# Optimization experiments

Hardware: AMD Instinct MI355X
Metric: run time of the kernel (lower is better)

## Reference

```python
import jax, jax.numpy as jnp
import numpy as np
from jax import lax

EPS = 1e-5
K, S = 7, 4  # patch size / stride, hard-coded in the torch module


def _bn(x, g, b):
    # inference BN with running_mean=0, running_var=1
    return x * (g / np.sqrt(1.0 + EPS)).reshape(1, -1, 1, 1) + b.reshape(1, -1, 1, 1)


def _conv2d(x, w, groups=1, pad=0):
    return lax.conv_general_dilated(
        x, w, (1, 1), [(pad, pad), (pad, pad)],
        dimension_numbers=("NCHW", "OIHW", "NCHW"), feature_group_count=groups)


def _dsconv(x, dw_w, g1, b1, pw_w, g2, b2):
    c_in = x.shape[1]
    y = jax.nn.relu(_bn(_conv2d(x, dw_w, groups=c_in, pad=1), g1, b1))
    y = jax.nn.relu(_bn(_conv2d(y, pw_w, groups=1, pad=0), g2, b2))
    return y


def _unfold(x, nph, npw):
    # torch .unfold(2,K,S).unfold(3,K,S) -> [N,C,nph,npw,K,K]
    idx_h = jnp.arange(nph)[:, None] * S + jnp.arange(K)[None, :]  # [nph,K]
    idx_w = jnp.arange(npw)[:, None] * S + jnp.arange(K)[None, :]  # [npw,K]
    p = x[:, :, idx_h, :]            # [N,C,nph,K,W]
    p = p[:, :, :, :, idx_w]         # [N,C,nph,K,npw,K]
    return p.transpose(0, 1, 2, 4, 3, 5)  # [N,C,nph,npw,K,K]


def setup_inputs() -> dict:
    key = jax.random.key(0)
    ks = jax.random.split(key, 16)
    N, C, H, W = 8, 128, 128, 128
    sc = lambda *s: 1.0 / np.sqrt(np.prod(s[1:])) if len(s) > 1 else 0.02
    d = {
        "exemplar": jax.random.normal(ks[0], (N, C, H, W), jnp.float32),
        "query": jax.random.normal(ks[1], (N, C, H, W), jnp.float32),
        "w_conv_e": jax.random.normal(ks[2], (C, C), jnp.float32) * (1.0 / np.sqrt(C)),
        "w_gate1": jax.random.normal(ks[3], (1, C), jnp.float32) * (1.0 / np.sqrt(C)),
        "w_gate2": jax.random.normal(ks[4], (1, C), jnp.float32) * (1.0 / np.sqrt(C)),
        "dw1_w": jax.random.normal(ks[5], (C, 1, 3, 3), jnp.float32) * (1.0 / 3.0),
        "bn1a_g": jnp.ones((C,), jnp.float32), "bn1a_b": jnp.zeros((C,), jnp.float32),
        "pw1_w": jax.random.normal(ks[6], (C, C, 1, 1), jnp.float32) * (1.0 / np.sqrt(C)),
        "bn1b_g": jnp.ones((C,), jnp.float32), "bn1b_b": jnp.zeros((C,), jnp.float32),
        "dwf_w": jax.random.normal(ks[7], (2 * C, 1, 3, 3), jnp.float32) * (1.0 / 3.0),
        "bnfa_g": jnp.ones((2 * C,), jnp.float32), "bnfa_b": jnp.zeros((2 * C,), jnp.float32),
        "pwf_w": jax.random.normal(ks[8], (C, 2 * C, 1, 1), jnp.float32) * (1.0 / np.sqrt(2 * C)),
        "bnfb_g": jnp.ones((C,), jnp.float32), "bnfb_b": jnp.zeros((C,), jnp.float32),
    }
    return d


def reference(exemplar, query, w_conv_e, w_gate1, w_gate2,
              dw1_w, bn1a_g, bn1a_b, pw1_w, bn1b_g, bn1b_b,
              dwf_w, bnfa_g, bnfa_b, pwf_w, bnfb_g, bnfb_b):
    N, C, H, W = query.shape
    nph = (H - K) // S + 1
    npw = (W - K) // S + 1
    npatch = nph * npw
    D = K * K  # 49

    ex_p = _unfold(exemplar, nph, npw)  # [N,C,nph,npw,K,K]
    q_p = _unfold(query, nph, npw)
    # faithful to torch: raw row-major reinterpretation [N,C,nph,npw,K,K] -> [N*npatch, C, D]
    ex_flat = ex_p.reshape(N * npatch, C, D)
    q_flat = q_p.reshape(N * npatch, C, D)

    ex_corr = jnp.einsum("oc,bcd->bod", w_conv_e, ex_flat)       # conv1d k=1
    A = jnp.einsum("bcd,bce->bde", ex_corr, q_flat)              # [B,D,D]
    A1 = jax.nn.softmax(A, axis=1)
    B2 = jax.nn.softmax(A, axis=2)                               # = softmax(A^T, dim=1) transposed back
    query_att = jnp.einsum("bcd,bde->bce", ex_flat, A1)          # [B,C,D]
    exemplar_att = jnp.einsum("bce,bde->bcd", q_flat, B2)        # [B,C,D]

    def recon(att):
        a = att.reshape(N, nph, npw, C, K, K)
        a = a.transpose(0, 3, 1, 4, 2, 5).reshape(N, C, nph * K, npw * K)
        return a[:, :, :H, :W]

    query_att = recon(query_att)
    exemplar_att = recon(exemplar_att)

    ex_mask = jax.nn.sigmoid(jnp.einsum("oc,nchw->nohw", w_gate1, exemplar_att))
    exemplar_att = exemplar_att * ex_mask
    exemplar_out = _dsconv(exemplar_att + exemplar, dw1_w, bn1a_g, bn1a_b, pw1_w, bn1b_g, bn1b_b)

    q_mask = jax.nn.sigmoid(jnp.einsum("oc,nchw->nohw", w_gate2, query_att))
    query_att = query_att * q_mask
    query_out = _dsconv(query_att + query, dw1_w, bn1a_g, bn1a_b, pw1_w, bn1b_g, bn1b_b)

    pred = _dsconv(jnp.concatenate([exemplar_out, query_out], axis=1),
                   dwf_w, bnfa_g, bnfa_b, pwf_w, bnfb_g, bnfb_b)
    return pred
```

## Files before the change

kernel.cpp:

```cpp
#include <hip/hip_runtime.h>
#include <hip/hip_bf16.h>

#define NN 8
#define CC 128
#define HH 128
#define WW 128
#define HWP (HH*WW)
#define KK 7
#define DD 49
#define NPH 31
#define NPATCH 961
#define PHN 19
#define PAD 52
#define PP2 (PAD*PAD)

typedef __attribute__((ext_vector_type(8))) short bf16x8;
typedef __attribute__((ext_vector_type(4))) float f32x4;
typedef __attribute__((ext_vector_type(4))) unsigned short us4;

__device__ __forceinline__ unsigned short f2bf(float f) {
    unsigned u = __builtin_bit_cast(unsigned, f);
    return (unsigned short)((u + 0x7FFFu + ((u >> 16) & 1u)) >> 16);
}

__global__ __launch_bounds__(512, 4) void attn_kernel(
    const float* __restrict__ ex_g, const float* __restrict__ q_g,
    const float* __restrict__ Wce, const float* __restrict__ wg1,
    const float* __restrict__ wg2,
    float* __restrict__ xe, float* __restrict__ xq)
{
    __shared__ float s_ex[CC*PAD];
    __shared__ float s_q [CC*PAD];
    __shared__ float s_scr[CC*PAD];
    __shared__ float s_m1[PAD], s_l1[PAD], s_m2[PAD], s_l2[PAD];
    __shared__ float s_g1[PAD], s_g2[PAD], s_me[PAD], s_mq[PAD];

    const int t  = threadIdx.x;
    const int n  = blockIdx.y;
    const int ph = blockIdx.x / PHN;
    const int pw = blockIdx.x % PHN;
    const int pp = (ph * NPH + pw) * CC;

    const float* exn = ex_g + (size_t)n * CC * HWP;
    const float* qn  = q_g  + (size_t)n * CC * HWP;

    #pragma unroll
    for (int ii = 0; ii < 2; ++ii) {
        const int i  = t + ii*512;
        const int c2 = i >> 3, kh = i & 7;
        const int rem  = pp + c2;
        const int c_u  = rem / NPATCH;
        const int p_u  = rem - c_u * NPATCH;
        const int ph_u = p_u / NPH;
        const int pw_u = p_u - ph_u * NPH;
        float* de = &s_ex[c2*PAD + kh*KK];
        if (kh < KK) {
            const float* se = exn + ((c_u*HH + ph_u*4 + kh)*WW + pw_u*4);
            const float4 e4 = *(const float4*)se;
            const float2 e2 = *(const float2*)(se + 4);
            const float  e1 = se[6];
            de[0]=e4.x; de[1]=e4.y; de[2]=e4.z; de[3]=e4.w;
            de[4]=e2.x; de[5]=e2.y; de[6]=e1;
        } else {
            de[0]=0.f; de[1]=0.f; de[2]=0.f;
        }
    }
    __syncthreads();

    if (t >= 64 && t < 480) {
        const int t2 = t - 64;
        const int eg_o = t2 / 13, eg_d = t2 - (t2/13)*13;
        const int o0 = eg_o*4, d0 = eg_d*4;
        float ac[4][4];
        #pragma unroll
        for (int i = 0; i < 4; ++i)
            #pragma unroll
            for (int j = 0; j < 4; ++j) ac[i][j] = 0.f;
        for (int k = 0; k < CC; k += 4) {
            float xm[4][4];
            #pragma unroll
            for (int kk = 0; kk < 4; ++kk) {
                float4 xv = *(const float4*)&s_ex[(k+kk)*PAD + d0];
                xm[kk][0]=xv.x; xm[kk][1]=xv.y; xm[kk][2]=xv.z; xm[kk][3]=xv.w;
            }
            #pragma unroll
            for (int i = 0; i < 4; ++i) {
                float4 wv = *(const float4*)&Wce[(o0+i)*CC + k];
                float wr[4] = {wv.x, wv.y, wv.z, wv.w};
                #pragma unroll
                for (int kk = 0; kk < 4; ++kk)
                    #pragma unroll
                    for (int j = 0; j < 4; ++j)
                        ac[i][j] = fmaf(wr[kk], xm[kk][j], ac[i][j]);
            }
        }
        #pragma unroll
        for (int i = 0; i < 4; ++i)
            *(float4*)&s_scr[(o0+i)*PAD + d0] =
                make_float4(ac[i][0], ac[i][1], ac[i][2], ac[i][3]);
    } else if (t < 64) {
        #pragma unroll 4
        for (int jj = 0; jj < 16; ++jj) {
            const int i  = t + jj*64;
            const int c2 = i >> 3, kh = i & 7;
            const int rem  = pp + c2;
            const int c_u  = rem / NPATCH;
            const int p_u  = rem - c_u * NPATCH;
            const int ph_u = p_u / NPH;
            const int pw_u = p_u - ph_u * NPH;
            float* dq = &s_q[c2*PAD + kh*KK];
            if (kh < KK) {
                const float* sq = qn + ((c_u*HH + ph_u*4 + kh)*WW + pw_u*4);
                const float4 q4 = *(const float4*)sq;
                const float2 q2 = *(const float2*)(sq + 4);
                const float  q1 = sq[6];
                dq[0]=q4.x; dq[1]=q4.y; dq[2]=q4.z; dq[3]=q4.w;
                dq[4]=q2.x; dq[5]=q2.y; dq[6]=q1;
            } else {
                dq[0]=0.f; dq[1]=0.f; dq[2]=0.f;
            }
        }
    }
    __syncthreads();

    float aa[4][2];
    int ad0 = 0, ae0 = 0;
    if (t < 338) {
        int dg = t % 13, eg = t / 13;
        ad0 = dg*4; ae0 = eg*2;
        #pragma unroll
        for (int i = 0; i < 4; ++i) { aa[i][0] = 0.f; aa[i][1] = 0.f; }
        #pragma unroll 4
        for (int k = 0; k < CC; ++k) {
            float4 ev = *(const float4*)&s_scr[k*PAD + ad0];
            float2 qv = *(const float2*)&s_q [k*PAD + ae0];
            #pragma unroll
            for (int i = 0; i < 4; ++i) {
                float e = (i==0)?ev.x:(i==1)?ev.y:(i==2)?ev.z:ev.w;
                aa[i][0] = fmaf(e, qv.x, aa[i][0]);
                aa[i][1] = fmaf(e, qv.y, aa[i][1]);
            }
        }
    } else if (t >= 352 && t < 352 + DD) {
        int e = t - 352;
        float acc = 0.f;
        for (int c = 0; c < CC; ++c) acc = fmaf(wg1[c], s_q[c*PAD + e], acc);
        s_g1[e] = acc;
    } else if (t >= 416 && t < 416 + DD) {
        int d = t - 416;
        float acc = 0.f;
        for (int c = 0; c < CC; ++c) acc = fmaf(wg2[c], s_ex[c*PAD + d], acc);
        s_g2[d] = acc;
    }
    __syncthreads();
    if (t < 338) {
        #pragma unroll
        for (int i = 0; i < 4; ++i)
            *(float2*)&s_scr[(ad0+i)*PAD + ae0] = make_float2(aa[i][0], aa[i][1]);
    }
    __syncthreads();

    {
        const int sub  = t & 3;
        const int line = (t >> 2) & 63;
        const int lo   = sub * 13;
        float v[13];
        if (t < 256) {
            if (line < DD) {
                #pragma unroll
                for (int j = 0; j < 13; ++j) {
                    int d = lo + j;
                    v[j] = (d < DD) ? s_scr[d*PAD + line] : -1e30f;
                }
                float m = v[0];
                #pragma unroll
                for (int j = 1; j < 13; ++j) m = fmaxf(m, v[j]);
                m = fmaxf(m, __shfl_xor(m, 1));
                m = fmaxf(m, __shfl_xor(m, 2));
                float l = 0.f;
                #pragma unroll
                for (int j = 0; j < 13; ++j) l += __expf(v[j] - m);
                l += __shfl_xor(l, 1);
                l += __shfl_xor(l, 2);
                if (sub == 0) { s_m1[line] = m; s_l1[line] = 1.f / l; }
            } else if (line < PAD && sub == 0) { s_m1[line] = 0.f; s_l1[line] = 0.f; }
        } else {
            if (line < DD) {
                #pragma unroll
                for (int j = 0; j < 13; ++j) {
                    int e = lo + j;
                    v[j] = (e < DD) ? s_scr[line*PAD + e] : -1e30f;
                }
                float m = v[0];
                #pragma unroll
                for (int j = 1; j < 13; ++j) m = fmaxf(m, v[j]);
                m = fmaxf(m, __shfl_xor(m, 1));
                m = fmaxf(m, __shfl_xor(m, 2));
                float l = 0.f;
                #pragma unroll
                for (int j = 0; j < 13; ++j) l += __expf(v[j] - m);
                l += __shfl_xor(l, 1);
                l += __shfl_xor(l, 2);
                if (sub == 0) { s_m2[line] = m; s_l2[line] = 1.f / l; }
            } else if (line < PAD && sub == 0) { s_m2[line] = 0.f; s_l2[line] = 0.f; }
        }
    }
    __syncthreads();

    float* P1  = s_scr + PP2;
    float* P2T = s_scr;
    {
        float p2buf[6]; int nv = 0;
        for (int i = t; i < PP2; i += 512) {
            int d = i / PAD, e = i - d*PAD;
            float a = s_scr[i];
            P1[i] = __expf(a - s_m1[e]) * s_l1[e];
            p2buf[nv++] = __expf(a - s_m2[d]) * s_l2[d];
        }
        __syncthreads();
        nv = 0;
        for (int i = t; i < PP2; i += 512) {
            int d = i / PAD, e = i - d*PAD;
            P2T[e*PAD + d] = p2buf[nv++];
        }
    }
    __syncthreads();

    float ae_[4][4], aq_[4][4];
    int c0 = 0, x0 = 0;
    if (t < 416) {
        int cg = t / 13, xg = t - (t/13)*13;
        c0 = cg*4; x0 = xg*4;
        #pragma unroll
        for (int i = 0; i < 4; ++i)
            #pragma unroll
            for (int j = 0; j < 4; ++j) { ae_[i][j] = 0.f; aq_[i][j] = 0.f; }
        for (int k = 0; k < 48; k += 4) {
            float qm[4][4], xm[4][4], p1m[4][4], p2m[4][4];
            #pragma unroll
            for (int i = 0; i < 4; ++i) {
                float4 qv = *(const float4*)&s_q [(c0+i)*PAD + k];
                float4 xv = *(const float4*)&s_ex[(c0+i)*PAD + k];
                qm[i][0]=qv.x; qm[i][1]=qv.y; qm[i][2]=qv.z; qm[i][3]=qv.w;
                xm[i][0]=xv.x; xm[i][1]=xv.y; xm[i][2]=xv.z; xm[i][3]=xv.w;
            }
            #pragma unroll
            for (int kk = 0; kk < 4; ++kk) {
                float4 p1 = *(const float4*)&P1 [(k+kk)*PAD + x0];
                float4 p2 = *(const float4*)&P2T[(k+kk)*PAD + x0];
                p1m[kk][0]=p1.x; p1m[kk][1]=p1.y; p1m[kk][2]=p1.z; p1m[kk][3]=p1.w;
                p2m[kk][0]=p2.x; p2m[kk][1]=p2.y; p2m[kk][2]=p2.z; p2m[kk][3]=p2.w;
            }
            #pragma unroll
            for (int kk = 0; kk < 4; ++kk)
                #pragma unroll
                for (int i = 0; i < 4; ++i)
                    #pragma unroll
                    for (int j = 0; j < 4; ++j) {
                        ae_[i][j] = fmaf(qm[i][kk], p2m[kk][j], ae_[i][j]);
                        aq_[i][j] = fmaf(xm[i][kk], p1m[kk][j], aq_[i][j]);
                    }
        }
        {
            const int k = 48;
            float p1r[4], p2r[4];
            #pragma unroll
            for (int j = 0; j < 4; ++j) { p1r[j] = P1 [k*PAD + x0 + j];
                                          p2r[j] = P2T[k*PAD + x0 + j]; }
            #pragma unroll
            for (int i = 0; i < 4; ++i) {
                float qv = s_q [(c0+i)*PAD + k];
                float xv = s_ex[(c0+i)*PAD + k];
                #pragma unroll
                for (int j = 0; j < 4; ++j) {
                    ae_[i][j] = fmaf(qv, p2r[j], ae_[i][j]);
                    aq_[i][j] = fmaf(xv, p1r[j], aq_[i][j]);
                }
            }
        }
    } else {
        const int u = t - 416;
        if (u < DD) {
            float a1 = 0.f;
            for (int e = 0; e < DD; ++e) a1 = fmaf(s_g1[e], P2T[e*PAD + u], a1);
            s_me[u] = 1.f / (1.f + __expf(-a1));
            if (u < 2) {
                const int e2 = DD - 2 + u;
                float a2 = 0.f;
                for (int d = 0; d < DD; ++d) a2 = fmaf(s_g2[d], P1[d*PAD + e2], a2);
                s_mq[e2] = 1.f / (1.f + __expf(-a2));
            }
        } else {
            const int e2 = u - DD;
            float a2 = 0.f;
            for (int d = 0; d < DD; ++d) a2 = fmaf(s_g2[d], P1[d*PAD + e2], a2);
            s_mq[e2] = 1.f / (1.f + __expf(-a2));
        }
    }
    __syncthreads();
    if (t < 416) {
        #pragma unroll
        for (int i = 0; i < 4; ++i) {
            *(float4*)&s_ex[(c0+i)*PAD + x0] =
                make_float4(ae_[i][0], ae_[i][1], ae_[i][2], ae_[i][3]);
            *(float4*)&s_q [(c0+i)*PAD + x0] =
                make_float4(aq_[i][0], aq_[i][1], aq_[i][2], aq_[i][3]);
        }
    }
    __syncthreads();

    {
        const size_t nbase = (size_t)n * CC * HWP;
        const int hb = ph*KK, wb = pw*KK;
        const int wlim = (WW - wb) < KK ? (WW - wb) : KK;
        #pragma unroll
        for (int ii = 0; ii < 2; ++ii) {
            const int i  = t + ii*512;
            const int c  = i >> 3, kh = i & 7;
            const int h  = hb + kh;
            if (kh < KK && h < HH) {
                const int li = (c*HH + h)*WW + wb;
                const float* sxe = &s_ex[c*PAD + kh*KK];
                const float* sxq = &s_q [c*PAD + kh*KK];
                if (wlim == KK) {
                    #pragma unroll
                    for (int kw = 0; kw < KK; ++kw) {
                        const int d = kh*KK + kw;
                        xe[nbase + li + kw] = sxe[kw]*s_me[d] + exn[li + kw];
                        xq[nbase + li + kw] = sxq[kw]*s_mq[d] + qn [li + kw];
                    }
                } else {
                    for (int kw = 0; kw < wlim; ++kw) {
                        const int d = kh*KK + kw;
                        xe[nbase + li + kw] = sxe[kw]*s_me[d] + exn[li + kw];
                        xq[nbase + li + kw] = sxq[kw]*s_mq[d] + qn [li + kw];
                    }
                }
            }
        }
    }
}

__global__ __launch_bounds__(256) void dw2_kernel(
    const float* __restrict__ xA, unsigned short* __restrict__ yA,
    const float* __restrict__ xB, unsigned short* __restrict__ yB,
    const float* __restrict__ wdw, const float* __restrict__ g,
    const float* __restrict__ b, int CoutTot, int coffA, int coffB)
{
    int bid = blockIdx.x;
    int sel = bid >> 12;
    int idx = (bid & 4095) * 256 + threadIdx.x;
    const float* x = sel ? xB : xA;
    unsigned short* y = sel ? yB : yA;
    int coff          = sel ? coffB : coffA;

    int w4 = (idx & 31) * 4;
    int h4 = ((idx >> 5) & 31) * 4;
    int nc = idx >> 10;
    int c  = nc & 127;
    int n  = nc >> 7;

    const float* wp = wdw + (coff + c) * 9;
    float wr[9];
    #pragma unroll
    for (int i = 0; i < 9; ++i) wr[i] = wp[i];

    const float* base = x + (size_t)nc * HWP;
    float acc[4][4];
    #pragma unroll
    for (int i = 0; i < 4; ++i)
        #pragma unroll
        for (int j = 0; j < 4; ++j) acc[i][j] = 0.f;

    #pragma unroll
    for (int r = 0; r < 6; ++r) {
        int hh = h4 - 1 + r;
        if (hh >= 0 && hh < HH) {
            const float* row = base + hh * WW + w4;
            float4 v = *(const float4*)row;
            float e[6];
            e[0] = (w4 > 0)   ? row[-1] : 0.f;
            e[1] = v.x; e[2] = v.y; e[3] = v.z; e[4] = v.w;
            e[5] = (w4 < 124) ? row[4]  : 0.f;
            int ilo = r - 2 > 0 ? r - 2 : 0;
            int ihi = r < 3 ? r : 3;
            for (int i = ilo; i <= ihi; ++i) {
                int j = r - i;
                float wa = wr[j*3], wb = wr[j*3+1], wc = wr[j*3+2];
                acc[i][0] += wa*e[0] + wb*e[1] + wc*e[2];
                acc[i][1] += wa*e[1] + wb*e[2] + wc*e[3];
                acc[i][2] += wa*e[2] + wb*e[3] + wc*e[4];
                acc[i][3] += wa*e[3] + wb*e[4] + wc*e[5];
            }
        }
    }
    const float rs = 0.99999500003749968f;
    float sc = g[coff + c] * rs, bi = b[coff + c];
    unsigned short* outp = y + (((size_t)n * CoutTot + coff + c) * HH + h4) * WW + w4;
    #pragma unroll
    for (int i = 0; i < 4; ++i) {
        us4 o;
        o[0] = f2bf(fmaxf(acc[i][0] * sc + bi, 0.f));
        o[1] = f2bf(fmaxf(acc[i][1] * sc + bi, 0.f));
        o[2] = f2bf(fmaxf(acc[i][2] * sc + bi, 0.f));
        o[3] = f2bf(fmaxf(acc[i][3] * sc + bi, 0.f));
        *(us4*)(outp + i * WW) = o;
    }
}

#define ZSTR 56

__global__ __launch_bounds__(256, 2) void pw_mfma_kernel(
    const unsigned short* __restrict__ zA, float* __restrict__ outA,
    const unsigned short* __restrict__ zB, float* __restrict__ outB,
    const float* __restrict__ Wp, const float* __restrict__ g,
    const float* __restrict__ b, int Cin)
{
    __shared__ unsigned short s_w[128*ZSTR];
    __shared__ unsigned short s_z[128*ZSTR];

    const int t  = threadIdx.x;
    const int n  = blockIdx.y;
    const int p0 = blockIdx.x * 128;
    const unsigned short* z = blockIdx.z ? zB : zA;
    float* out              = blockIdx.z ? outB : outA;

    const int wave = t >> 6, lane = t & 63;
    const int wo  = (wave & 1) * 64;
    const int wp_ = (wave >> 1) * 64;
    const int lm  = lane & 15, lq = lane >> 4;

    f32x4 acc[4][4];
    #pragma unroll
    for (int i = 0; i < 4; ++i)
        #pragma unroll
        for (int j = 0; j < 4; ++j)
            #pragma unroll
            for (int r = 0; r < 4; ++r) acc[i][j][r] = 0.f;

    const unsigned short* zn = z + (size_t)n * Cin * HWP;

    for (int kb = 0; kb < Cin; kb += 32) {
        {
            int o = t >> 1, cb = (t & 1) * 16;
            const float* wrow = Wp + o * Cin + kb + cb;
            unsigned short* dst = s_w + o * ZSTR + cb;
            #pragma unroll
            for (int i = 0; i < 16; i += 4) {
                float4 v = *(const float4*)(wrow + i);
                dst[i+0] = f2bf(v.x); dst[i+1] = f2bf(v.y);
                dst[i+2] = f2bf(v.z); dst[i+3] = f2bf(v.w);
            }
        }
        {
            int cc = t & 31, pxg = (t >> 5) * 16;
            const unsigned short* src = zn + (size_t)(kb + cc) * HWP + p0 + pxg;
            uint4 a = *(const uint4*)src;
            uint4 b2 = *(const uint4*)(src + 8);
            unsigned v[8] = {a.x, a.y, a.z, a.w, b2.x, b2.y, b2.z, b2.w};
            #pragma unroll
            for (int i = 0; i < 8; ++i) {
                s_z[(pxg + 2*i    ) * ZSTR + cc] = (unsigned short)(v[i] & 0xffffu);
                s_z[(pxg + 2*i + 1) * ZSTR + cc] = (unsigned short)(v[i] >> 16);
            }
        }
        __syncthreads();

        bf16x8 af[4], bfv[4];
        #pragma unroll
        for (int i = 0; i < 4; ++i)
            af[i] = *(const bf16x8*)&s_w[(wo + i*16 + lm) * ZSTR + lq*8];
        #pragma unroll
        for (int j = 0; j < 4; ++j)
            bfv[j] = *(const bf16x8*)&s_z[(wp_ + j*16 + lm) * ZSTR + lq*8];
        #pragma unroll
        for (int i = 0; i < 4; ++i)
            #pragma unroll
            for (int j = 0; j < 4; ++j)
                acc[i][j] = __builtin_amdgcn_mfma_f32_16x16x32_bf16(
                    af[i], bfv[j], acc[i][j], 0, 0, 0);
        __syncthreads();
    }

    const float rs = 0.99999500003749968f;
    float* on = out + (size_t)n * 128 * HWP;
    #pragma unroll
    for (int i = 0; i < 4; ++i) {
        #pragma unroll
        for (int r = 0; r < 4; ++r) {
            int o = wo + i*16 + lq*4 + r;
            float sc = g[o] * rs, bi = b[o];
            #pragma unroll
            for (int j = 0; j < 4; ++j) {
                int px = wp_ + j*16 + lm;
                on[(size_t)o * HWP + p0 + px] =
                    fmaxf(acc[i][j][r] * sc + bi, 0.f);
            }
        }
    }
}

extern "C" void kernel_launch(void* const* d_in, const int* in_sizes, int n_in,
                              void* d_out, int out_size, void* d_ws, size_t ws_size,
                              hipStream_t stream) {
    const float* exemplar = (const float*)d_in[0];
    const float* query    = (const float*)d_in[1];
    const float* w_conv_e = (const float*)d_in[2];
    const float* w_gate1  = (const float*)d_in[3];
    const float* w_gate2  = (const float*)d_in[4];
    const float* dw1_w    = (const float*)d_in[5];
    const float* bn1a_g   = (const float*)d_in[6];
    const float* bn1a_b   = (const float*)d_in[7];
    const float* pw1_w    = (const float*)d_in[8];
    const float* bn1b_g   = (const float*)d_in[9];
    const float* bn1b_b   = (const float*)d_in[10];
    const float* dwf_w    = (const float*)d_in[11];
    const float* bnfa_g   = (const float*)d_in[12];
    const float* bnfa_b   = (const float*)d_in[13];
    const float* pwf_w    = (const float*)d_in[14];
    const float* bnfb_g   = (const float*)d_in[15];
    const float* bnfb_b   = (const float*)d_in[16];

    float* out = (float*)d_out;
    float* ws  = (float*)d_ws;
    const size_t SZ = (size_t)NN * CC * HWP;
    float* bufA = ws;
    float* bufB = ws + SZ;
    unsigned short* zE  = (unsigned short*)(ws + 2*SZ);
    unsigned short* zQ  = zE + SZ;
    unsigned short* T16 = (unsigned short*)(ws + 3*SZ);

    attn_kernel<<<dim3(PHN * PHN, NN), 512, 0, stream>>>(
        exemplar, query, w_conv_e, w_gate1, w_gate2, bufA, bufB);

    dw2_kernel<<<8192, 256, 0, stream>>>(bufA, zE, bufB, zQ,
                                         dw1_w, bn1a_g, bn1a_b, 128, 0, 0);

    pw_mfma_kernel<<<dim3(128, NN, 2), 256, 0, stream>>>(
        zE, bufA, zQ, bufB, pw1_w, bn1b_g, bn1b_b, 128);

    dw2_kernel<<<8192, 256, 0, stream>>>(bufA, T16, bufB, T16,
                                         dwf_w, bnfa_g, bnfa_b, 256, 0, 128);

    pw_mfma_kernel<<<dim3(128, NN, 1), 256, 0, stream>>>(
        T16, out, (const unsigned short*)nullptr, (float*)nullptr,
        pwf_w, bnfb_g, bnfb_b, 256);
}
```

Baseline: 669.3 us.

## Compute patch attention products with bf16 MFMA and fold gate masks into stores

Replaces the scalar fp32 4x4 register-tiled products of the exemplar/query patches with the softmax matrices in the attention kernel with bf16 16x16x32 MFMA instructions. The operands are converted to bf16 in padded shared-memory tiles, and the sigmoid gate masks are applied in the shared-memory writeback instead of during the global store. The pointwise conv kernel's launch bounds are also raised to request 3 blocks per CU. This cuts the ALU work of the attention step, at the cost of bf16 rounding of the softmax probabilities and activations, extra conversion and zero-padding passes, and possible register pressure from the occupancy hint.

```diff
diff --git a/kernel.cpp b/kernel.cpp
--- a/kernel.cpp
+++ b/kernel.cpp
@@ -13,6 +13,7 @@
 #define PHN 19
 #define PAD 52
 #define PP2 (PAD*PAD)
+#define XSTR 72
 
 typedef __attribute__((ext_vector_type(8))) short bf16x8;
 typedef __attribute__((ext_vector_type(4))) float f32x4;
@@ -21,6 +22,9 @@
 __device__ __forceinline__ unsigned short f2bf(float f) {
     unsigned u = __builtin_bit_cast(unsigned, f);
     return (unsigned short)((u + 0x7FFFu + ((u >> 16) & 1u)) >> 16);
+}
+__device__ __forceinline__ float bf2f(unsigned short u) {
+    return __builtin_bit_cast(float, (unsigned)u << 16);
 }
 
 __global__ __launch_bounds__(512, 4) void attn_kernel(
@@ -160,6 +164,13 @@
     }
     __syncthreads();
 
+    float cex[13], cq[13];
+    #pragma unroll
+    for (int k = 0; k < 13; ++k) {
+        int i = t + k*512;
+        cex[k] = s_ex[i];
+        cq[k]  = s_q[i];
+    }
     {
         const int sub  = t & 3;
         const int line = (t >> 2) & 63;
@@ -207,104 +218,106 @@
     }
     __syncthreads();
 
-    float* P1  = s_scr + PP2;
-    float* P2T = s_scr;
-    {
-        float p2buf[6]; int nv = 0;
-        for (int i = t; i < PP2; i += 512) {
+    unsigned short* exh = (unsigned short*)s_ex;
+    unsigned short* qh  = (unsigned short*)s_q;
+    float p1v[6], p2v[6];
+    #pragma unroll
+    for (int k = 0; k < 13; ++k) {
+        int i = t + k*512;
+        int c = i / PAD, d = i - c*PAD;
+        exh[c*XSTR + d] = f2bf(cex[k]);
+        qh [c*XSTR + d] = f2bf(cq[k]);
+    }
+    for (int i = t; i < CC*12; i += 512) {
+        int c = i / 12, d = 52 + (i - (i/12)*12);
+        exh[c*XSTR + d] = 0;
+        qh [c*XSTR + d] = 0;
+    }
+    #pragma unroll
+    for (int k = 0; k < 6; ++k) {
+        int i = t + k*512;
+        if (i < PP2) {
             int d = i / PAD, e = i - d*PAD;
             float a = s_scr[i];
-            P1[i] = __expf(a - s_m1[e]) * s_l1[e];
-            p2buf[nv++] = __expf(a - s_m2[d]) * s_l2[d];
-        }
-        __syncthreads();
-        nv = 0;
-        for (int i = t; i < PP2; i += 512) {
+            p1v[k] = __expf(a - s_m1[e]) * s_l1[e];
+            p2v[k] = __expf(a - s_m2[d]) * s_l2[d];
+        }
+    }
+    __syncthreads();
+
+    unsigned short* p2h = (unsigned short*)s_scr;
+    unsigned short* p1t = p2h + 64*XSTR;
+    #pragma unroll
+    for (int k = 0; k < 6; ++k) {
+        int i = t + k*512;
+        if (i < PP2) {
             int d = i / PAD, e = i - d*PAD;
-            P2T[e*PAD + d] = p2buf[nv++];
-        }
-    }
-    __syncthreads();
-
-    float ae_[4][4], aq_[4][4];
-    int c0 = 0, x0 = 0;
-    if (t < 416) {
-        int cg = t / 13, xg = t - (t/13)*13;
-        c0 = cg*4; x0 = xg*4;
-        #pragma unroll
-        for (int i = 0; i < 4; ++i)
-            #pragma unroll
-            for (int j = 0; j < 4; ++j) { ae_[i][j] = 0.f; aq_[i][j] = 0.f; }
-        for (int k = 0; k < 48; k += 4) {
-            float qm[4][4], xm[4][4], p1m[4][4], p2m[4][4];
-            #pragma unroll
-            for (int i = 0; i < 4; ++i) {
-                float4 qv = *(const float4*)&s_q [(c0+i)*PAD + k];
-                float4 xv = *(const float4*)&s_ex[(c0+i)*PAD + k];
-                qm[i][0]=qv.x; qm[i][1]=qv.y; qm[i][2]=qv.z; qm[i][3]=qv.w;
-                xm[i][0]=xv.x; xm[i][1]=xv.y; xm[i][2]=xv.z; xm[i][3]=xv.w;
-            }
-            #pragma unroll
-            for (int kk = 0; kk < 4; ++kk) {
-                float4 p1 = *(const float4*)&P1 [(k+kk)*PAD + x0];
-                float4 p2 = *(const float4*)&P2T[(k+kk)*PAD + x0];
-                p1m[kk][0]=p1.x; p1m[kk][1]=p1.y; p1m[kk][2]=p1.z; p1m[kk][3]=p1.w;
-                p2m[kk][0]=p2.x; p2m[kk][1]=p2.y; p2m[kk][2]=p2.z; p2m[kk][3]=p2.w;
-            }
-            #pragma unroll
-            for (int kk = 0; kk < 4; ++kk)
-                #pragma unroll
-                for (int i = 0; i < 4; ++i)
-                    #pragma unroll
-                    for (int j = 0; j < 4; ++j) {
-                        ae_[i][j] = fmaf(qm[i][kk], p2m[kk][j], ae_[i][j]);
-                        aq_[i][j] = fmaf(xm[i][kk], p1m[kk][j], aq_[i][j]);
-                    }
-        }
-        {
-            const int k = 48;
-            float p1r[4], p2r[4];
-            #pragma unroll
-            for (int j = 0; j < 4; ++j) { p1r[j] = P1 [k*PAD + x0 + j];
-                                          p2r[j] = P2T[k*PAD + x0 + j]; }
-            #pragma unroll
-            for (int i = 0; i < 4; ++i) {
-                float qv = s_q [(c0+i)*PAD + k];
-                float xv = s_ex[(c0+i)*PAD + k];
-                #pragma unroll
-                for (int j = 0; j < 4; ++j) {
-                    ae_[i][j] = fmaf(qv, p2r[j], ae_[i][j]);
-                    aq_[i][j] = fmaf(xv, p1r[j], aq_[i][j]);
-                }
-            }
-        }
-    } else {
-        const int u = t - 416;
-        if (u < DD) {
-            float a1 = 0.f;
-            for (int e = 0; e < DD; ++e) a1 = fmaf(s_g1[e], P2T[e*PAD + u], a1);
-            s_me[u] = 1.f / (1.f + __expf(-a1));
-            if (u < 2) {
-                const int e2 = DD - 2 + u;
-                float a2 = 0.f;
-                for (int d = 0; d < DD; ++d) a2 = fmaf(s_g2[d], P1[d*PAD + e2], a2);
-                s_mq[e2] = 1.f / (1.f + __expf(-a2));
-            }
-        } else {
-            const int e2 = u - DD;
-            float a2 = 0.f;
-            for (int d = 0; d < DD; ++d) a2 = fmaf(s_g2[d], P1[d*PAD + e2], a2);
-            s_mq[e2] = 1.f / (1.f + __expf(-a2));
-        }
-    }
-    __syncthreads();
-    if (t < 416) {
-        #pragma unroll
-        for (int i = 0; i < 4; ++i) {
-            *(float4*)&s_ex[(c0+i)*PAD + x0] =
-                make_float4(ae_[i][0], ae_[i][1], ae_[i][2], ae_[i][3]);
-            *(float4*)&s_q [(c0+i)*PAD + x0] =
-                make_float4(aq_[i][0], aq_[i][1], aq_[i][2], aq_[i][3]);
+            if (d < DD && e < DD) {
+                p2h[d*XSTR + e] = f2bf(p2v[k]);
+                p1t[e*XSTR + d] = f2bf(p1v[k]);
+            }
+        }
+    }
+    for (int i = t; i < DD*15; i += 512) {
+        int r = i / 15, c2 = 49 + (i - (i/15)*15);
+        p2h[r*XSTR + c2] = 0;
+        p1t[r*XSTR + c2] = 0;
+    }
+    __syncthreads();
+
+    const int wv  = t >> 6, lane = t & 63;
+    const int lm0 = lane & 15, lq = lane >> 4;
+    const int crow = wv*16 + lm0;
+    f32x4 accQ[4], accE[4];
+    #pragma unroll
+    for (int nt = 0; nt < 4; ++nt)
+        #pragma unroll
+        for (int r = 0; r < 4; ++r) { accQ[nt][r] = 0.f; accE[nt][r] = 0.f; }
+    {
+        bf16x8 ax[2], aq2[2];
+        ax[0]  = *(const bf16x8*)&exh[crow*XSTR + lq*8];
+        ax[1]  = *(const bf16x8*)&exh[crow*XSTR + 32 + lq*8];
+        aq2[0] = *(const bf16x8*)&qh [crow*XSTR + lq*8];
+        aq2[1] = *(const bf16x8*)&qh [crow*XSTR + 32 + lq*8];
+        #pragma unroll
+        for (int nt = 0; nt < 4; ++nt) {
+            const int brow = nt*16 + lm0;
+            #pragma unroll
+            for (int ks = 0; ks < 2; ++ks) {
+                bf16x8 b1 = *(const bf16x8*)&p1t[brow*XSTR + ks*32 + lq*8];
+                bf16x8 b2 = *(const bf16x8*)&p2h[brow*XSTR + ks*32 + lq*8];
+                accQ[nt] = __builtin_amdgcn_mfma_f32_16x16x32_bf16(
+                    ax[ks],  b1, accQ[nt], 0, 0, 0);
+                accE[nt] = __builtin_amdgcn_mfma_f32_16x16x32_bf16(
+                    aq2[ks], b2, accE[nt], 0, 0, 0);
+            }
+        }
+    }
+    if (t < DD) {
+        float a1 = 0.f;
+        for (int e = 0; e < DD; ++e)
+            a1 = fmaf(s_g1[e], bf2f(p2h[t*XSTR + e]), a1);
+        s_me[t] = 1.f / (1.f + __expf(-a1));
+    } else if (t >= 64 && t < 64 + DD) {
+        int e2 = t - 64;
+        float a2 = 0.f;
+        for (int d = 0; d < DD; ++d)
+            a2 = fmaf(s_g2[d], bf2f(p1t[e2*XSTR + d]), a2);
+        s_mq[e2] = 1.f / (1.f + __expf(-a2));
+    }
+    __syncthreads();
+
+    #pragma unroll
+    for (int nt = 0; nt < 4; ++nt) {
+        const int col = nt*16 + lm0;
+        if (col < DD) {
+            const float me_ = s_me[col], mq_ = s_mq[col];
+            #pragma unroll
+            for (int r = 0; r < 4; ++r) {
+                const int c = wv*16 + lq*4 + r;
+                s_ex[c*PAD + col] = accE[nt][r] * me_;
+                s_q [c*PAD + col] = accQ[nt][r] * mq_;
+            }
         }
     }
     __syncthreads();
@@ -325,15 +338,13 @@
                 if (wlim == KK) {
                     #pragma unroll
                     for (int kw = 0; kw < KK; ++kw) {
-                        const int d = kh*KK + kw;
-                        xe[nbase + li + kw] = sxe[kw]*s_me[d] + exn[li + kw];
-                        xq[nbase + li + kw] = sxq[kw]*s_mq[d] + qn [li + kw];
+                        xe[nbase + li + kw] = sxe[kw] + exn[li + kw];
+                        xq[nbase + li + kw] = sxq[kw] + qn [li + kw];
                     }
                 } else {
                     for (int kw = 0; kw < wlim; ++kw) {
-                        const int d = kh*KK + kw;
-                        xe[nbase + li + kw] = sxe[kw]*s_me[d] + exn[li + kw];
-                        xq[nbase + li + kw] = sxq[kw]*s_mq[d] + qn [li + kw];
+                        xe[nbase + li + kw] = sxe[kw] + exn[li + kw];
+                        xq[nbase + li + kw] = sxq[kw] + qn [li + kw];
                     }
                 }
             }
@@ -410,7 +421,7 @@
 
 #define ZSTR 56
 
-__global__ __launch_bounds__(256, 2) void pw_mfma_kernel(
+__global__ __launch_bounds__(256, 3) void pw_mfma_kernel(
     const unsigned short* __restrict__ zA, float* __restrict__ outA,
     const unsigned short* __restrict__ zB, float* __restrict__ outB,
     const float* __restrict__ Wp, const float* __restrict__ g,
```

Result: faster. 635.8 us (-5.0%).
